# Kernel optimization log

Hardware: AMD Instinct MI355X
Metric: run time of the kernel (lower is better)

The kernel has to match this reference:

```python
import jax, jax.numpy as jnp
import numpy as np


def setup_inputs() -> dict:
    key = jax.random.key(0)
    k1, k2, k3 = jax.random.split(key, 3)
    B, S, D_IN, D_OUT = 4, 2048, 4096, 4096
    x = jax.random.normal(k1, (B, S, D_IN), dtype=jnp.float32)
    # int8 quantized weight [out_features, in_features], values in [-127, 127]
    weight_q = jax.random.randint(k2, (D_OUT, D_IN), -127, 128, dtype=jnp.int32).astype(jnp.int8)
    # per-tensor symmetric scale, shape [1]
    scale = jax.random.uniform(k3, (1,), dtype=jnp.float32, minval=0.01, maxval=0.05)
    return {"x": x, "weight_q": weight_q, "scale": scale}


def reference(x, weight_q, scale):
    # scale_dequantize: upcast int8 weight to input dtype, multiply by scale
    w = weight_q.astype(x.dtype) * scale  # [out, in]
    # F.linear(input, weight): y = x @ w.T
    return jnp.einsum('bsi,oi->bso', x, w)
```

## Files before the change

### kernel.cpp

```cpp
#include <hip/hip_runtime.h>
#include <hip/hip_bf16.h>
#include <stdint.h>


#define M_DIM 8192
#define N_DIM 4096
#define K_DIM 4096
#define BM 256
#define BN 256
#define BK 64
#define NT (K_DIM / BK)

typedef __attribute__((ext_vector_type(4))) float    f32x4;
typedef __attribute__((ext_vector_type(4))) int      i32x4;
typedef __attribute__((ext_vector_type(2))) uint32_t u32x2;
typedef __attribute__((ext_vector_type(4))) uint32_t u32x4;
typedef __attribute__((ext_vector_type(8))) short    bf16x8;
typedef uint32_t u32;

__device__ __forceinline__ u32 fbits(float f) { return __builtin_bit_cast(u32, f); }
__device__ __forceinline__ u32 pack_bf16_trunc(float lo, float hi) {
    return __builtin_amdgcn_perm(fbits(hi), fbits(lo), 0x07060302u);
}
__device__ __forceinline__ int swzb(int row, int bytecol) {
    return row * 128 + (bytecol ^ ((row & 7) << 4));
}

__device__ __forceinline__ void gload_lds16(const void* g, void* s) {
    __builtin_amdgcn_global_load_lds(
        (const __attribute__((address_space(1))) void*)(uintptr_t)g,
        (__attribute__((address_space(3))) void*)(u32)(uintptr_t)s, 16, 0, 0);
}

#define WAIT_VM4()   do { asm volatile("s_waitcnt vmcnt(4)" ::: "memory");   \
                          __builtin_amdgcn_sched_barrier(0); } while (0)
#define WAIT_VM0()   do { asm volatile("s_waitcnt vmcnt(0)" ::: "memory");   \
                          __builtin_amdgcn_sched_barrier(0); } while (0)
#define BARRIER()    do { __builtin_amdgcn_s_barrier();                      \
                          __builtin_amdgcn_sched_barrier(0); } while (0)

#define NXB ((M_DIM * K_DIM) / (8 * 256))
#define NWB ((N_DIM * K_DIM) / (8 * 256))
__global__ __launch_bounds__(256)
void qlin_convert_xw(const float* __restrict__ X, const int* __restrict__ Wq,
                     short* __restrict__ Xb, short* __restrict__ Wb)
{
    const int b = (int)blockIdx.x;
    if (b < NXB) {
        const size_t i = (size_t)b * 256 + threadIdx.x;
        f32x4 a = ((const f32x4*)X)[2 * i];
        f32x4 c = ((const f32x4*)X)[2 * i + 1];
        u32x4 q;
        q[0] = pack_bf16_trunc(a[0], a[1]);
        q[1] = pack_bf16_trunc(a[2], a[3]);
        q[2] = pack_bf16_trunc(c[0], c[1]);
        q[3] = pack_bf16_trunc(c[2], c[3]);
        ((u32x4*)Xb)[i] = q;
    } else {
        const size_t i = (size_t)(b - NXB) * 256 + threadIdx.x;
        i32x4 w0 = ((const i32x4*)Wq)[2 * i];
        i32x4 w1 = ((const i32x4*)Wq)[2 * i + 1];
        u32x4 q;
        q[0] = pack_bf16_trunc((float)w0[0], (float)w0[1]);
        q[1] = pack_bf16_trunc((float)w0[2], (float)w0[3]);
        q[2] = pack_bf16_trunc((float)w1[0], (float)w1[1]);
        q[3] = pack_bf16_trunc((float)w1[2], (float)w1[3]);
        ((u32x4*)Wb)[i] = q;
    }
}

__global__ __launch_bounds__(512, 2)
void qlin_gemm_p(const short* __restrict__ A, const short* __restrict__ B,
                 const float* __restrict__ scale_p, float* __restrict__ C)
{
    __shared__ __align__(16) char As[2][2][128 * 128];
    __shared__ __align__(16) char Bs[3][2][128 * 128];

    const int tid = threadIdx.x;
    const int nwg = (M_DIM / BM) * (N_DIM / BN);
    const int cpx = nwg / 8;
    const int bid = ((int)blockIdx.x % 8) * cpx + (int)blockIdx.x / 8;
    const int tileM = (bid / (N_DIM / BN)) * BM;
    const int tileN = (bid % (N_DIM / BN)) * BN;

    const int lane = tid & 63;
    const int wid  = tid >> 6;
    const int wr   = wid >> 2;
    const int wc   = wid & 3;
    const int lr   = lane & 15;
    const int lq   = lane >> 4;

    const int srow = lane >> 3;
    const int scol = ((lane & 7) ^ srow) << 4;
    const char* Ag = (const char*)A;
    const char* Bg = (const char*)B;

    auto stageA = [&](int buf, int h, int kt) {
#pragma unroll
        for (int j = 0; j < 2; ++j) {
            const int seg = wid * 2 + j;
            const char* src = Ag + (size_t)(tileM + h * 128 + seg * 8 + srow) * (K_DIM * 2)
                                 + kt * (BK * 2) + scol;
            gload_lds16(src, &As[buf][h][seg * 1024]);
        }
    };
    auto stageB = [&](int buf, int h, int kt) {
#pragma unroll
        for (int j = 0; j < 2; ++j) {
            const int seg = wid * 2 + j;
            const char* src = Bg + (size_t)(tileN + h * 128 + seg * 8 + srow) * (K_DIM * 2)
                                 + kt * (BK * 2) + scol;
            gload_lds16(src, &Bs[buf][h][seg * 1024]);
        }
    };

    f32x4  acc[8][4] = {};
    bf16x8 afr[4][2];
    bf16x8 b0fr[2][2], b2fr[2][2];

    auto swzh = [](int row, int bc) { return row * 128 + (bc ^ ((row & 7) << 4)); };
    auto ldA = [&](int buf, int mb) {
#pragma unroll
        for (int m = 0; m < 4; ++m) {
            const int row = (mb + m) * 16 + lr;
#pragma unroll
            for (int ks = 0; ks < 2; ++ks)
                afr[m][ks] = *(const bf16x8*)&As[buf][wr][swzh(row, ks * 64 + lq * 16)];
        }
    };
    auto ldB = [&](int buf, int nb, bf16x8 (&bf)[2][2]) {
#pragma unroll
        for (int n = 0; n < 2; ++n) {
            const int r = wc * 64 + (nb + n) * 16 + lr;
#pragma unroll
            for (int ks = 0; ks < 2; ++ks)
                bf[n][ks] = *(const bf16x8*)&Bs[buf][r >> 7][swzh(r & 127, ks * 64 + lq * 16)];
        }
    };
    auto quad = [&](int mb, int nb, bf16x8 (&bf)[2][2]) {
        __builtin_amdgcn_s_setprio(1);
#pragma unroll
        for (int ks = 0; ks < 2; ++ks)
#pragma unroll
            for (int m = 0; m < 4; ++m)
#pragma unroll
                for (int n = 0; n < 2; ++n)
                    acc[mb + m][nb + n] = __builtin_amdgcn_mfma_f32_16x16x32_bf16(
                        afr[m][ks], bf[n][ks], acc[mb + m][nb + n], 0, 0, 0);
        __builtin_amdgcn_s_setprio(0);
    };

    stageA(0, 0, 0); stageA(0, 1, 0);
    stageB(0, 0, 0); stageB(0, 1, 0);
    stageB(1, 0, 1); stageB(1, 1, 1);
    WAIT_VM4();
    BARRIER();

    int curB = 0, preB = 2;
#pragma unroll 1
    for (int kt = 0; kt < NT; ++kt) {
        const int curA = kt & 1, nxtA = curA ^ 1;

        ldA(curA, 0);
        ldB(curB, 0, b0fr);
        ldB(curB, 2, b2fr);
        if (kt + 1 < NT) { stageA(nxtA, 0, kt + 1); stageA(nxtA, 1, kt + 1); }

        quad(0, 0, b0fr);
        quad(0, 2, b2fr);

        ldA(curA, 4);
        if (kt + 2 < NT) { stageB(preB, 0, kt + 2); stageB(preB, 1, kt + 2); }

        quad(4, 2, b2fr);
        quad(4, 0, b0fr);

        if (kt + 2 < NT)      { WAIT_VM4(); }
        else if (kt + 1 < NT) { WAIT_VM0(); }
        BARRIER();

        curB = (curB == 2) ? 0 : curB + 1;
        preB = (preB == 2) ? 0 : preB + 1;
    }

    const float scl = scale_p[0];
#pragma unroll
    for (int m = 0; m < 8; ++m) {
        const int gm0 = tileM + wr * 128 + m * 16 + lq * 4;
#pragma unroll
        for (int n = 0; n < 4; ++n) {
            const int gn = tileN + wc * 64 + n * 16 + lr;
            float* cp = C + (size_t)gm0 * N_DIM + gn;
#pragma unroll
            for (int r = 0; r < 4; ++r)
                cp[(size_t)r * N_DIM] = acc[m][n][r] * scl;
        }
    }
}

#define TILE_BYTES (BM * BK * 2)
__global__ __launch_bounds__(512, 2)
void qlin_gemm8(const void* __restrict__ Asrc, const void* __restrict__ Bsrc,
                const float* __restrict__ scale_p, float* __restrict__ C)
{
    __shared__ char As[2 * TILE_BYTES];
    __shared__ char Bs[2 * TILE_BYTES];

    const int tid = threadIdx.x;
    const int nwg = (M_DIM / BM) * (N_DIM / BN);
    const int cpx = nwg / 8;
    const int bid = ((int)blockIdx.x % 8) * cpx + (int)blockIdx.x / 8;
    const int tileM = (bid / (N_DIM / BN)) * BM;
    const int tileN = (bid % (N_DIM / BN)) * BN;

    const int lane = tid & 63;
    const int wid  = tid >> 6;
    const int wr   = wid >> 2;
    const int wc   = wid & 3;
    const int lr   = lane & 15;
    const int lq   = lane >> 4;

    f32x4  aF[8]; i32x4 wF[8];

    const float* ag0 = (const float*)Asrc + (size_t)(tileM + (tid >> 4)) * K_DIM + (tid & 15) * 4;
    const int*   bg0 = (const int*)Bsrc  + (size_t)(tileN + (tid >> 4)) * K_DIM + (tid & 15) * 4;

    auto stage_load = [&](int kt) {
#pragma unroll
        for (int i = 0; i < 8; ++i)
            aF[i] = *(const f32x4*)(ag0 + (size_t)(32 * i) * K_DIM + kt * BK);
#pragma unroll
        for (int i = 0; i < 8; ++i)
            wF[i] = *(const i32x4*)(bg0 + (size_t)(32 * i) * K_DIM + kt * BK);
    };
    auto stage_writeA = [&](int nxt) {
        char* dst = As + nxt * TILE_BYTES;
#pragma unroll
        for (int i = 0; i < 8; ++i) {
            u32x2 p;
            p[0] = pack_bf16_trunc(aF[i][0], aF[i][1]);
            p[1] = pack_bf16_trunc(aF[i][2], aF[i][3]);
            *(u32x2*)(dst + swzb((tid >> 4) + 32 * i, (tid & 15) * 8)) = p;
        }
    };
    auto stage_writeB = [&](int nxt) {
        char* dst = Bs + nxt * TILE_BYTES;
#pragma unroll
        for (int i = 0; i < 8; ++i) {
            u32x2 p;
            p[0] = pack_bf16_trunc((float)wF[i][0], (float)wF[i][1]);
            p[1] = pack_bf16_trunc((float)wF[i][2], (float)wF[i][3]);
            *(u32x2*)(dst + swzb((tid >> 4) + 32 * i, (tid & 15) * 8)) = p;
        }
    };

    f32x4  acc[8][4] = {};
    bf16x8 afr[4][2], bfr[2][2];

    auto ldA = [&](const char* buf, int mb) {
#pragma unroll
        for (int m = 0; m < 4; ++m) {
            const int row = wr * 128 + (mb + m) * 16 + lr;
#pragma unroll
            for (int ks = 0; ks < 2; ++ks)
                afr[m][ks] = *(const bf16x8*)(buf + swzb(row, ks * 64 + lq * 16));
        }
    };
    auto ldB = [&](const char* buf, int nb) {
#pragma unroll
        for (int n = 0; n < 2; ++n) {
            const int row = wc * 64 + (nb + n) * 16 + lr;
#pragma unroll
            for (int ks = 0; ks < 2; ++ks)
                bfr[n][ks] = *(const bf16x8*)(buf + swzb(row, ks * 64 + lq * 16));
        }
    };
    auto quad = [&](int mb, int nb) {
        __builtin_amdgcn_s_setprio(1);
#pragma unroll
        for (int ks = 0; ks < 2; ++ks)
#pragma unroll
            for (int m = 0; m < 4; ++m)
#pragma unroll
                for (int n = 0; n < 2; ++n)
                    acc[mb + m][nb + n] = __builtin_amdgcn_mfma_f32_16x16x32_bf16(
                        afr[m][ks], bfr[n][ks], acc[mb + m][nb + n], 0, 0, 0);
        __builtin_amdgcn_s_setprio(0);
    };

    stage_load(0);
    stage_writeA(0);
    stage_writeB(0);
    __syncthreads();

#pragma unroll 1
    for (int kt = 0; kt < NT; ++kt) {
        const int cur = kt & 1, nxt = cur ^ 1;
        const bool more = (kt + 1) < NT;
        const char* Ab = As + cur * TILE_BYTES;
        const char* Bb = Bs + cur * TILE_BYTES;

        if (more) stage_load(kt + 1);

        ldA(Ab, 0); ldB(Bb, 0); quad(0, 0);
        ldB(Bb, 2);             quad(0, 2);
        ldA(Ab, 4);
        if (more) stage_writeA(nxt);
        quad(4, 2);
        ldB(Bb, 0);
        if (more) stage_writeB(nxt);
        quad(4, 0);

        __syncthreads();
    }

    const float scl = scale_p[0];
#pragma unroll
    for (int m = 0; m < 8; ++m) {
        const int gm0 = tileM + wr * 128 + m * 16 + lq * 4;
#pragma unroll
        for (int n = 0; n < 4; ++n) {
            const int gn = tileN + wc * 64 + n * 16 + lr;
            float* cp = C + (size_t)gm0 * N_DIM + gn;
#pragma unroll
            for (int r = 0; r < 4; ++r)
                cp[(size_t)r * N_DIM] = acc[m][n][r] * scl;
        }
    }
}

extern "C" void kernel_launch(void* const* d_in, const int* in_sizes, int n_in,
                              void* d_out, int out_size, void* d_ws, size_t ws_size,
                              hipStream_t stream)
{
    (void)in_sizes; (void)n_in; (void)out_size;
    const float* X     = (const float*)d_in[0];
    const int*   Wq    = (const int*)d_in[1];
    const float* scale = (const float*)d_in[2];
    float* C = (float*)d_out;

    const size_t xbytes = (size_t)M_DIM * K_DIM * sizeof(short);
    const size_t wbytes = (size_t)N_DIM * K_DIM * sizeof(short);

    if (ws_size >= xbytes + wbytes) {
        short* Xb = (short*)d_ws;
        short* Wb = (short*)((char*)d_ws + xbytes);
        qlin_convert_xw<<<dim3(NXB + NWB), dim3(256), 0, stream>>>(X, Wq, Xb, Wb);
        qlin_gemm_p<<<dim3((M_DIM / BM) * (N_DIM / BN)), dim3(512), 0, stream>>>(Xb, Wb, scale, C);
    } else {
        qlin_gemm8<<<dim3((M_DIM / BM) * (N_DIM / BN)), dim3(512), 0, stream>>>(X, Wq, scale, C);
    }
}
```

Measured before the change: 261.8 us.

## Make GEMM persistent over two M tiles per workgroup with continuous pipeline

```diff
diff --git a/kernel.cpp b/kernel.cpp
--- a/kernel.cpp
+++ b/kernel.cpp
@@ -77,11 +77,11 @@
     __shared__ __align__(16) char Bs[3][2][128 * 128];
 
     const int tid = threadIdx.x;
-    const int nwg = (M_DIM / BM) * (N_DIM / BN);
-    const int cpx = nwg / 8;
-    const int bid = ((int)blockIdx.x % 8) * cpx + (int)blockIdx.x / 8;
-    const int tileM = (bid / (N_DIM / BN)) * BM;
-    const int tileN = (bid % (N_DIM / BN)) * BN;
+    const int r  = (int)blockIdx.x;
+    const int t0 = (r & 7) * 64 + (r >> 3);
+    const int tileN  = (t0 & 15) * BN;
+    const int tileM0 = (t0 >> 4) * BM;
+    const int tileM1 = tileM0 + 2 * BM;
 
     const int lane = tid & 63;
     const int wid  = tid >> 6;
@@ -95,21 +95,24 @@
     const char* Ag = (const char*)A;
     const char* Bg = (const char*)B;
 
-    auto stageA = [&](int buf, int h, int kt) {
+    auto stageA = [&](int buf, int h, int k) {
+        const int tm = (k >= NT) ? tileM1 : tileM0;
+        const int kk = k & (NT - 1);
 #pragma unroll
         for (int j = 0; j < 2; ++j) {
             const int seg = wid * 2 + j;
-            const char* src = Ag + (size_t)(tileM + h * 128 + seg * 8 + srow) * (K_DIM * 2)
-                                 + kt * (BK * 2) + scol;
+            const char* src = Ag + (size_t)(tm + h * 128 + seg * 8 + srow) * (K_DIM * 2)
+                                 + kk * (BK * 2) + scol;
             gload_lds16(src, &As[buf][h][seg * 1024]);
         }
     };
-    auto stageB = [&](int buf, int h, int kt) {
+    auto stageB = [&](int buf, int h, int k) {
+        const int kk = k & (NT - 1);
 #pragma unroll
         for (int j = 0; j < 2; ++j) {
             const int seg = wid * 2 + j;
             const char* src = Bg + (size_t)(tileN + h * 128 + seg * 8 + srow) * (K_DIM * 2)
-                                 + kt * (BK * 2) + scol;
+                                 + kk * (BK * 2) + scol;
             gload_lds16(src, &Bs[buf][h][seg * 1024]);
         }
     };
@@ -131,10 +134,10 @@
     auto ldB = [&](int buf, int nb, bf16x8 (&bf)[2][2]) {
 #pragma unroll
         for (int n = 0; n < 2; ++n) {
-            const int r = wc * 64 + (nb + n) * 16 + lr;
+            const int rr = wc * 64 + (nb + n) * 16 + lr;
 #pragma unroll
             for (int ks = 0; ks < 2; ++ks)
-                bf[n][ks] = *(const bf16x8*)&Bs[buf][r >> 7][swzh(r & 127, ks * 64 + lq * 16)];
+                bf[n][ks] = *(const bf16x8*)&Bs[buf][rr >> 7][swzh(rr & 127, ks * 64 + lq * 16)];
         }
     };
     auto quad = [&](int mb, int nb, bf16x8 (&bf)[2][2]) {
@@ -148,6 +151,22 @@
                     acc[mb + m][nb + n] = __builtin_amdgcn_mfma_f32_16x16x32_bf16(
                         afr[m][ks], bf[n][ks], acc[mb + m][nb + n], 0, 0, 0);
         __builtin_amdgcn_s_setprio(0);
+    };
+
+    const float scl = scale_p[0];
+    auto epi = [&](int tm) {
+#pragma unroll
+        for (int m = 0; m < 8; ++m) {
+            const int gm0 = tm + wr * 128 + m * 16 + lq * 4;
+#pragma unroll
+            for (int n = 0; n < 4; ++n) {
+                const int gn = tileN + wc * 64 + n * 16 + lr;
+                float* cp = C + (size_t)gm0 * N_DIM + gn;
+#pragma unroll
+                for (int rr = 0; rr < 4; ++rr)
+                    cp[(size_t)rr * N_DIM] = acc[m][n][rr] * scl;
+            }
+        }
     };
 
     stageA(0, 0, 0); stageA(0, 1, 0);
@@ -158,44 +177,44 @@
 
     int curB = 0, preB = 2;
 #pragma unroll 1
-    for (int kt = 0; kt < NT; ++kt) {
-        const int curA = kt & 1, nxtA = curA ^ 1;
+    for (int k = 0; k < 2 * NT; ++k) {
+        const int curA = k & 1, nxtA = curA ^ 1;
+
+        if (k == NT) {
+            epi(tileM0);
+#pragma unroll
+            for (int m = 0; m < 8; ++m)
+#pragma unroll
+                for (int n = 0; n < 4; ++n)
+                    acc[m][n] = (f32x4){0.f, 0.f, 0.f, 0.f};
+        }
 
         ldA(curA, 0);
         ldB(curB, 0, b0fr);
         ldB(curB, 2, b2fr);
-        if (kt + 1 < NT) { stageA(nxtA, 0, kt + 1); stageA(nxtA, 1, kt + 1); }
+        if (k + 1 < 2 * NT) { stageA(nxtA, 0, k + 1); stageA(nxtA, 1, k + 1); }
 
         quad(0, 0, b0fr);
         quad(0, 2, b2fr);
 
         ldA(curA, 4);
-        if (kt + 2 < NT) { stageB(preB, 0, kt + 2); stageB(preB, 1, kt + 2); }
+        if (k + 2 < 2 * NT) { stageB(preB, 0, k + 2); stageB(preB, 1, k + 2); }
+
+        if (k + 2 < 2 * NT)      { WAIT_VM4(); }
+        else if (k + 1 < 2 * NT) { WAIT_VM0(); }
+        else {  }
 
         quad(4, 2, b2fr);
         quad(4, 0, b0fr);
 
-        if (kt + 2 < NT)      { WAIT_VM4(); }
-        else if (kt + 1 < NT) { WAIT_VM0(); }
+        if (k + 2 >= 2 * NT && k + 1 < 2 * NT) { }
         BARRIER();
 
         curB = (curB == 2) ? 0 : curB + 1;
         preB = (preB == 2) ? 0 : preB + 1;
     }
 
-    const float scl = scale_p[0];
-#pragma unroll
-    for (int m = 0; m < 8; ++m) {
-        const int gm0 = tileM + wr * 128 + m * 16 + lq * 4;
-#pragma unroll
-        for (int n = 0; n < 4; ++n) {
-            const int gn = tileN + wc * 64 + n * 16 + lr;
-            float* cp = C + (size_t)gm0 * N_DIM + gn;
-#pragma unroll
-            for (int r = 0; r < 4; ++r)
-                cp[(size_t)r * N_DIM] = acc[m][n][r] * scl;
-        }
-    }
+    epi(tileM1);
 }
 
 #define TILE_BYTES (BM * BK * 2)
@@ -323,8 +342,8 @@
             const int gn = tileN + wc * 64 + n * 16 + lr;
             float* cp = C + (size_t)gm0 * N_DIM + gn;
 #pragma unroll
-            for (int r = 0; r < 4; ++r)
-                cp[(size_t)r * N_DIM] = acc[m][n][r] * scl;
+            for (int rr = 0; rr < 4; ++rr)
+                cp[(size_t)rr * N_DIM] = acc[m][n][rr] * scl;
         }
     }
 }
@@ -346,7 +365,7 @@
         short* Xb = (short*)d_ws;
         short* Wb = (short*)((char*)d_ws + xbytes);
         qlin_convert_xw<<<dim3(NXB + NWB), dim3(256), 0, stream>>>(X, Wq, Xb, Wb);
-        qlin_gemm_p<<<dim3((M_DIM / BM) * (N_DIM / BN)), dim3(512), 0, stream>>>(Xb, Wb, scale, C);
+        qlin_gemm_p<<<dim3(256), dim3(512), 0, stream>>>(Xb, Wb, scale, C);
     } else {
         qlin_gemm8<<<dim3((M_DIM / BM) * (N_DIM / BN)), dim3(512), 0, stream>>>(X, Wq, scale, C);
     }
```

Result: slower. 447.0 us (+70.8%).
